# Kernel tuning notes

Hardware: AMD Instinct MI355X
Metric: run time of the kernel (lower is better)

The kernel has to match this reference:

```python
import jax, jax.numpy as jnp
import numpy as np

N_NODES = 100000
N_EDGES = 3200000
IN_F = 128
HEADS = 8
OUT_C = 2  # GATConv out_channels hardcoded to 2 in the source
NEG_SLOPE = 0.2  # PyG GATConv default leaky_relu slope


def setup_inputs() -> dict:
    key = jax.random.key(0)
    ks = jax.random.split(key, 9)
    x = jax.random.normal(ks[0], (N_NODES, IN_F), dtype=jnp.float32)
    edge_index = jax.random.randint(ks[1], (2, N_EDGES), 0, N_NODES, dtype=jnp.int64)
    edge_attr = jax.random.uniform(ks[2], (N_EDGES, 1), dtype=jnp.float32)
    s = 1.0 / np.sqrt(IN_F)
    W = jax.random.normal(ks[3], (IN_F, HEADS * OUT_C), dtype=jnp.float32) * s
    att_src = jax.random.normal(ks[4], (HEADS, OUT_C), dtype=jnp.float32) * 0.5
    att_dst = jax.random.normal(ks[5], (HEADS, OUT_C), dtype=jnp.float32) * 0.5
    bias_gat = jnp.zeros((HEADS * OUT_C,), dtype=jnp.float32)
    W_fc = jax.random.normal(ks[6], (HEADS * OUT_C, 2), dtype=jnp.float32) * 0.25
    b_fc = jnp.zeros((2,), dtype=jnp.float32)
    return {"x": x, "edge_index": edge_index, "edge_attr": edge_attr,
            "W": W, "att_src": att_src, "att_dst": att_dst,
            "bias_gat": bias_gat, "W_fc": W_fc, "b_fc": b_fc}


def reference(x, edge_index, edge_attr, W, att_src, att_dst, bias_gat, W_fc, b_fc):
    # edge_attr is ignored: GATConv was built without edge_dim, matching the source.
    N = x.shape[0]
    # PyG GATConv adds self-loops by default
    loops = jnp.arange(N, dtype=edge_index.dtype)
    src = jnp.concatenate([edge_index[0], loops])  # [E']
    dst = jnp.concatenate([edge_index[1], loops])  # [E']

    h = (x @ W).reshape(N, HEADS, OUT_C)                 # [N,H,C]
    a_src = jnp.einsum('nhc,hc->nh', h, att_src)          # [N,H]
    a_dst = jnp.einsum('nhc,hc->nh', h, att_dst)          # [N,H]

    logits = jax.nn.leaky_relu(a_src[src] + a_dst[dst], negative_slope=NEG_SLOPE)  # [E',H]
    # segment softmax over edges grouped by destination node (self-loops ensure non-empty segments)
    seg_max = jax.ops.segment_max(logits, dst, num_segments=N)   # [N,H]
    p = jnp.exp(logits - seg_max[dst])                            # [E',H]
    seg_sum = jax.ops.segment_sum(p, dst, num_segments=N)         # [N,H]
    alpha = p / seg_sum[dst]                                      # [E',H]

    msg = alpha[:, :, None] * h[src]                              # [E',H,C]
    agg = jax.ops.segment_sum(msg, dst, num_segments=N)           # [N,H,C]
    gat_out = agg.reshape(N, HEADS * OUT_C) + bias_gat            # concat heads + bias
    return gat_out @ W_fc + b_fc                                  # [N,2]
```

## Files before the change

kernel.cpp:

```cpp
#include <hip/hip_runtime.h>
#include <hip/hip_fp16.h>

#define N_NODES 100000
#define IN_F 128
#define NF 16
#define HEADS 8
#define NEG_SLOPE 0.2f
#define LOG2E 1.44269504f

#define RB 256
#define LOG_RB 8
#define NB 391
#define SBITS 17
#define SMASK ((1u << SBITS) - 1)
#define BIN_C 4096
#define CAPB 9024


__device__ __forceinline__ void phase1_body(
    int pb, const float* __restrict__ x, const float* __restrict__ W,
    __half* __restrict__ rec, float* Ws)
{
    int t = threadIdx.x;
    for (int i = t; i < IN_F * NF; i += 512) Ws[i] = W[i];
    __syncthreads();

    int tid  = pb * 512 + t;
    int node = tid >> 4;
    int j    = tid & 15;
    if (node >= N_NODES) return;

    const float4* xr4 = (const float4*)(x + (size_t)node * IN_F);
    float acc0 = 0.f, acc1 = 0.f;
    #pragma unroll 8
    for (int k4 = 0; k4 < IN_F / 4; k4 += 2) {
        float4 xa = xr4[k4];
        float4 xb = xr4[k4 + 1];
        acc0 = fmaf(xa.x, Ws[(4 * k4 + 0) * NF + j], acc0);
        acc0 = fmaf(xa.y, Ws[(4 * k4 + 1) * NF + j], acc0);
        acc0 = fmaf(xa.z, Ws[(4 * k4 + 2) * NF + j], acc0);
        acc0 = fmaf(xa.w, Ws[(4 * k4 + 3) * NF + j], acc0);
        acc1 = fmaf(xb.x, Ws[(4 * k4 + 4) * NF + j], acc1);
        acc1 = fmaf(xb.y, Ws[(4 * k4 + 5) * NF + j], acc1);
        acc1 = fmaf(xb.z, Ws[(4 * k4 + 6) * NF + j], acc1);
        acc1 = fmaf(xb.w, Ws[(4 * k4 + 7) * NF + j], acc1);
    }
    rec[(size_t)node * NF + j] = __float2half(acc0 + acc1);
}

__global__ __launch_bounds__(512) void fused_p1_bin(
    const int* __restrict__ ei, int* __restrict__ bin_cursor,
    unsigned* __restrict__ bins,
    const float* __restrict__ x, const float* __restrict__ W,
    __half* __restrict__ rec, int E, int SB)
{
    __shared__ union {
        struct {
            unsigned staging[BIN_C];
            unsigned short bin16[BIN_C];
            int hist[NB], offs[NB], cur[NB], gbase[NB];
            int wsum[8], woff[8];
        } b;
        float Ws[IN_F * NF];
    } sm;

    int idx = blockIdx.x;
    bool is_bin = (idx % 5 == 0) && (idx / 5 < SB);
    if (!is_bin) {
        int cb = (idx + 4) / 5; if (cb > SB) cb = SB;
        phase1_body(idx - cb, x, W, rec, sm.Ws);
        return;
    }

    int t = threadIdx.x;
    int base = (idx / 5) * BIN_C;
    int n_valid = E - base;
    if (n_valid > BIN_C) n_valid = BIN_C;
    if (n_valid < 0) n_valid = 0;

    int es[8], ed[8];
    #pragma unroll
    for (int k = 0; k < 8; ++k) {
        int i = t + 512 * k;
        bool v = i < n_valid;
        es[k] = v ? ei[base + i] : 0;
        ed[k] = v ? ei[E + base + i] : -1;
    }

    if (t < NB) sm.b.hist[t] = 0;
    __syncthreads();

    #pragma unroll
    for (int k = 0; k < 8; ++k)
        if (ed[k] >= 0) atomicAdd(&sm.b.hist[ed[k] >> LOG_RB], 1);
    __syncthreads();

    int sum = (t < NB) ? sm.b.hist[t] : 0;
    int lane = t & 63, wid = t >> 6;
    int v = sum;
    #pragma unroll
    for (int o = 1; o < 64; o <<= 1) {
        int u = __shfl_up(v, o);
        if (lane >= o) v += u;
    }
    if (lane == 63) sm.b.wsum[wid] = v;
    __syncthreads();
    if (t == 0) { int r = 0; for (int w = 0; w < 8; ++w) { sm.b.woff[w] = r; r += sm.b.wsum[w]; } }
    __syncthreads();
    int run = sm.b.woff[wid] + v - sum;
    if (t < NB) { sm.b.offs[t] = run; sm.b.cur[t] = run; }
    __syncthreads();
    if (t < NB)
        sm.b.gbase[t] = sm.b.hist[t] ? atomicAdd(&bin_cursor[t], sm.b.hist[t]) : 0;
    __syncthreads();

    #pragma unroll
    for (int k = 0; k < 8; ++k) {
        if (ed[k] >= 0) {
            int b = ed[k] >> LOG_RB;
            int slot = atomicAdd(&sm.b.cur[b], 1);
            sm.b.staging[slot] = ((unsigned)(ed[k] & (RB - 1)) << SBITS) | (unsigned)es[k];
            sm.b.bin16[slot] = (unsigned short)b;
        }
    }
    __syncthreads();

    for (int i = t; i < n_valid; i += 512) {
        int b = sm.b.bin16[i];
        int pos = sm.b.gbase[b] + (i - sm.b.offs[b]);
        if (pos < CAPB) bins[(size_t)b * CAPB + pos] = sm.b.staging[i];
    }
}

__global__ __launch_bounds__(1024) void accum6_kernel(
    const unsigned* __restrict__ bins, const int* __restrict__ bin_cursor,
    const __half* __restrict__ rec,
    const float* __restrict__ att_src, const float* __restrict__ att_dst,
    const float* __restrict__ bias, const float* __restrict__ Wfc,
    const float* __restrict__ bfc, float* __restrict__ out)
{
    __shared__ unsigned staging[CAPB];
    __shared__ int hist[RB], offs[RB + 1], cur[RB];

    int t = threadIdx.x;
    int b = blockIdx.x;
    int node0 = b * RB;

    if (t < RB) hist[t] = 0;
    __syncthreads();

    int cnt = bin_cursor[b];
    if (cnt > CAPB) cnt = CAPB;
    const unsigned* seg = bins + (size_t)b * CAPB;

    unsigned rcache[9];
    int nk = 0;
    for (int i = t; i < cnt; i += 1024) rcache[nk++] = seg[i];

    for (int k = 0; k < nk; ++k)
        atomicAdd(&hist[rcache[k] >> SBITS], 1);
    __syncthreads();

    if (t < 64) {
        int h0 = hist[4 * t], h1 = hist[4 * t + 1];
        int h2 = hist[4 * t + 2], h3 = hist[4 * t + 3];
        int v = h0 + h1 + h2 + h3;
        int inc = v;
        #pragma unroll
        for (int o = 1; o < 64; o <<= 1) {
            int u = __shfl_up(inc, o);
            if (t >= o) inc += u;
        }
        int ex = inc - v;
        offs[4 * t] = ex;     cur[4 * t] = ex;     ex += h0;
        offs[4 * t + 1] = ex; cur[4 * t + 1] = ex; ex += h1;
        offs[4 * t + 2] = ex; cur[4 * t + 2] = ex; ex += h2;
        offs[4 * t + 3] = ex; cur[4 * t + 3] = ex;
        if (t == 63) offs[RB] = inc;
    }
    __syncthreads();

    for (int k = 0; k < nk; ++k) {
        unsigned r = rcache[k];
        int slot = atomicAdd(&cur[r >> SBITS], 1);
        staging[slot] = r & SMASK;
    }
    __syncthreads();

    int wv = t >> 6, lane = t & 63;
    int h_id = lane & 7, e_off = lane >> 3;

    float as0 = att_src[2 * h_id] * LOG2E, as1 = att_src[2 * h_id + 1] * LOG2E;
    float ad0 = att_dst[2 * h_id] * LOG2E, ad1 = att_dst[2 * h_id + 1] * LOG2E;
    float b0 = bias[2 * h_id], b1 = bias[2 * h_id + 1];
    float w00 = Wfc[(2 * h_id) * 2 + 0],     w01 = Wfc[(2 * h_id) * 2 + 1];
    float w10 = Wfc[(2 * h_id + 1) * 2 + 0], w11 = Wfc[(2 * h_id + 1) * 2 + 1];
    float c0 = bfc[0], c1 = bfc[1];

    for (int k = 0; k < RB / 16; ++k) {
        int ln = wv + 16 * k;
        int n = node0 + ln;
        if (n >= N_NODES) break;
        int st  = offs[ln];
        int deg = offs[ln + 1] - st;

        __half2 hn = *(const __half2*)(rec + (size_t)n * NF + 2 * h_id);
        float hn0 = __half2float(hn.x), hn1 = __half2float(hn.y);
        float adst_h = ad0 * hn0 + ad1 * hn1;

        float den = 0.f, num0 = 0.f, num1 = 0.f;

        for (int i = e_off; i < deg; i += 8) {
            int s = staging[st + i];
            __half2 hs = *(const __half2*)(rec + (size_t)s * NF + 2 * h_id);
            float h0 = __half2float(hs.x), h1 = __half2float(hs.y);
            float l = fmaf(as0, h0, fmaf(as1, h1, adst_h));
            l = l > 0.f ? l : NEG_SLOPE * l;
            float p = exp2f(l);
            den += p;
            num0 = fmaf(p, h0, num0);
            num1 = fmaf(p, h1, num1);
        }
        #pragma unroll
        for (int m = 8; m < 64; m <<= 1) {
            den  += __shfl_xor(den,  m);
            num0 += __shfl_xor(num0, m);
            num1 += __shfl_xor(num1, m);
        }
        {
            float l = fmaf(as0, hn0, fmaf(as1, hn1, adst_h));
            l = l > 0.f ? l : NEG_SLOPE * l;
            float p = exp2f(l);
            den += p;
            num0 = fmaf(p, hn0, num0);
            num1 = fmaf(p, hn1, num1);
        }
        float g0 = num0 / den + b0;
        float g1 = num1 / den + b1;
        float o0 = g0 * w00 + g1 * w10;
        float o1 = g0 * w01 + g1 * w11;
        #pragma unroll
        for (int m = 1; m < 8; m <<= 1) {
            o0 += __shfl_xor(o0, m);
            o1 += __shfl_xor(o1, m);
        }
        if (lane == 0) {
            float2 res = { o0 + c0, o1 + c1 };
            *(float2*)(out + (size_t)n * 2) = res;
        }
    }
}

extern "C" void kernel_launch(void* const* d_in, const int* in_sizes, int n_in,
                              void* d_out, int out_size, void* d_ws, size_t ws_size,
                              hipStream_t stream)
{
    const float* x       = (const float*)d_in[0];
    const int*   ei      = (const int*)d_in[1];
    const float* W       = (const float*)d_in[3];
    const float* att_src = (const float*)d_in[4];
    const float* att_dst = (const float*)d_in[5];
    const float* bias    = (const float*)d_in[6];
    const float* Wfc     = (const float*)d_in[7];
    const float* bfc     = (const float*)d_in[8];
    float*       out     = (float*)d_out;

    const int E  = in_sizes[1] / 2;
    const int SB = (E + BIN_C - 1) / BIN_C;
    const int PB = (N_NODES * 16 + 511) / 512;

    __half* rec        = (__half*)d_ws;
    int*    bin_cursor = (int*)((char*)d_ws + (size_t)N_NODES * NF * 2);
    size_t  bins_off   = (((size_t)((char*)bin_cursor - (char*)d_ws)) + NB * 4 + 4095) & ~(size_t)4095;
    unsigned* bins     = (unsigned*)((char*)d_ws + bins_off);

    hipMemsetAsync(bin_cursor, 0, NB * sizeof(int), stream);

    fused_p1_bin<<<SB + PB, 512, 0, stream>>>(
        ei, bin_cursor, bins, x, W, rec, E, SB);
    accum6_kernel<<<NB, 1024, 0, stream>>>(
        bins, bin_cursor, rec, att_src, att_dst, bias, Wfc, bfc, out);
}
```

Measured before the change: 210.7 us.

## Halve projection threads per node, rebalance block interleave, unroll edge gather loop

```diff
diff --git a/kernel.cpp b/kernel.cpp
--- a/kernel.cpp
+++ b/kernel.cpp
@@ -26,26 +26,28 @@
     __syncthreads();
 
     int tid  = pb * 512 + t;
-    int node = tid >> 4;
-    int j    = tid & 15;
+    int node = tid >> 3;
+    int j    = tid & 7;
     if (node >= N_NODES) return;
 
     const float4* xr4 = (const float4*)(x + (size_t)node * IN_F);
-    float acc0 = 0.f, acc1 = 0.f;
+    const float2* Wp  = (const float2*)Ws;
+
+    float a0 = 0.f, b0 = 0.f, a1 = 0.f, b1 = 0.f;
     #pragma unroll 8
-    for (int k4 = 0; k4 < IN_F / 4; k4 += 2) {
-        float4 xa = xr4[k4];
-        float4 xb = xr4[k4 + 1];
-        acc0 = fmaf(xa.x, Ws[(4 * k4 + 0) * NF + j], acc0);
-        acc0 = fmaf(xa.y, Ws[(4 * k4 + 1) * NF + j], acc0);
-        acc0 = fmaf(xa.z, Ws[(4 * k4 + 2) * NF + j], acc0);
-        acc0 = fmaf(xa.w, Ws[(4 * k4 + 3) * NF + j], acc0);
-        acc1 = fmaf(xb.x, Ws[(4 * k4 + 4) * NF + j], acc1);
-        acc1 = fmaf(xb.y, Ws[(4 * k4 + 5) * NF + j], acc1);
-        acc1 = fmaf(xb.z, Ws[(4 * k4 + 6) * NF + j], acc1);
-        acc1 = fmaf(xb.w, Ws[(4 * k4 + 7) * NF + j], acc1);
-    }
-    rec[(size_t)node * NF + j] = __float2half(acc0 + acc1);
+    for (int k4 = 0; k4 < IN_F / 4; ++k4) {
+        float4 xv = xr4[k4];
+        float2 w0 = Wp[(4 * k4 + 0) * 8 + j];
+        float2 w1 = Wp[(4 * k4 + 1) * 8 + j];
+        float2 w2 = Wp[(4 * k4 + 2) * 8 + j];
+        float2 w3 = Wp[(4 * k4 + 3) * 8 + j];
+        a0 = fmaf(xv.x, w0.x, a0); b0 = fmaf(xv.x, w0.y, b0);
+        a1 = fmaf(xv.y, w1.x, a1); b1 = fmaf(xv.y, w1.y, b1);
+        a0 = fmaf(xv.z, w2.x, a0); b0 = fmaf(xv.z, w2.y, b0);
+        a1 = fmaf(xv.w, w3.x, a1); b1 = fmaf(xv.w, w3.y, b1);
+    }
+    __half2 hv = __floats2half2_rn(a0 + a1, b0 + b1);
+    *(__half2*)(rec + (size_t)node * NF + 2 * j) = hv;
 }
 
 __global__ __launch_bounds__(512) void fused_p1_bin(
@@ -65,15 +67,15 @@
     } sm;
 
     int idx = blockIdx.x;
-    bool is_bin = (idx % 5 == 0) && (idx / 5 < SB);
+    bool is_bin = (idx % 3 == 0) && (idx / 3 < SB);
     if (!is_bin) {
-        int cb = (idx + 4) / 5; if (cb > SB) cb = SB;
+        int cb = (idx + 2) / 3; if (cb > SB) cb = SB;
         phase1_body(idx - cb, x, W, rec, sm.Ws);
         return;
     }
 
     int t = threadIdx.x;
-    int base = (idx / 5) * BIN_C;
+    int base = (idx / 3) * BIN_C;
     int n_valid = E - base;
     if (n_valid > BIN_C) n_valid = BIN_C;
     if (n_valid < 0) n_valid = 0;
@@ -132,7 +134,7 @@
     }
 }
 
-__global__ __launch_bounds__(1024) void accum6_kernel(
+__global__ __launch_bounds__(1024) void accum7_kernel(
     const unsigned* __restrict__ bins, const int* __restrict__ bin_cursor,
     const __half* __restrict__ rec,
     const float* __restrict__ att_src, const float* __restrict__ att_dst,
@@ -209,8 +211,30 @@
         float adst_h = ad0 * hn0 + ad1 * hn1;
 
         float den = 0.f, num0 = 0.f, num1 = 0.f;
-
-        for (int i = e_off; i < deg; i += 8) {
+        float denB = 0.f, num0B = 0.f, num1B = 0.f;
+
+        int i = e_off;
+        for (; i + 8 < deg; i += 16) {
+            int sA = staging[st + i];
+            int sB = staging[st + i + 8];
+            __half2 hsA = *(const __half2*)(rec + (size_t)sA * NF + 2 * h_id);
+            __half2 hsB = *(const __half2*)(rec + (size_t)sB * NF + 2 * h_id);
+            float hA0 = __half2float(hsA.x), hA1 = __half2float(hsA.y);
+            float lA = fmaf(as0, hA0, fmaf(as1, hA1, adst_h));
+            lA = lA > 0.f ? lA : NEG_SLOPE * lA;
+            float pA = exp2f(lA);
+            den += pA;
+            num0 = fmaf(pA, hA0, num0);
+            num1 = fmaf(pA, hA1, num1);
+            float hB0 = __half2float(hsB.x), hB1 = __half2float(hsB.y);
+            float lB = fmaf(as0, hB0, fmaf(as1, hB1, adst_h));
+            lB = lB > 0.f ? lB : NEG_SLOPE * lB;
+            float pB = exp2f(lB);
+            denB += pB;
+            num0B = fmaf(pB, hB0, num0B);
+            num1B = fmaf(pB, hB1, num1B);
+        }
+        if (i < deg) {
             int s = staging[st + i];
             __half2 hs = *(const __half2*)(rec + (size_t)s * NF + 2 * h_id);
             float h0 = __half2float(hs.x), h1 = __half2float(hs.y);
@@ -221,6 +245,8 @@
             num0 = fmaf(p, h0, num0);
             num1 = fmaf(p, h1, num1);
         }
+        den += denB; num0 += num0B; num1 += num1B;
+
         #pragma unroll
         for (int m = 8; m < 64; m <<= 1) {
             den  += __shfl_xor(den,  m);
@@ -267,7 +293,7 @@
 
     const int E  = in_sizes[1] / 2;
     const int SB = (E + BIN_C - 1) / BIN_C;
-    const int PB = (N_NODES * 16 + 511) / 512;
+    const int PB = (N_NODES * 8 + 511) / 512;
 
     __half* rec        = (__half*)d_ws;
     int*    bin_cursor = (int*)((char*)d_ws + (size_t)N_NODES * NF * 2);
@@ -278,6 +304,6 @@
 
     fused_p1_bin<<<SB + PB, 512, 0, stream>>>(
         ei, bin_cursor, bins, x, W, rec, E, SB);
-    accum6_kernel<<<NB, 1024, 0, stream>>>(
+    accum7_kernel<<<NB, 1024, 0, stream>>>(
         bins, bin_cursor, rec, att_src, att_dst, bias, Wfc, bfc, out);
 }
```

Result: faster. 203.4 us (-3.5%).
